# Kernel tuning notes

Hardware: AMD Instinct MI355X
Metric: run time of the kernel (lower is better)

Reference implementation:

```python
import jax, jax.numpy as jnp
import numpy as np

N_NODES = 40000
N_EDGES = 640000
NUM_GRAPHS = 64
NODE_DIM = 128
EDGE_DIM = 32
HID = 64
AGG_HID = 128
NEG_SLOPE = 0.2


def _segment_softmax(logits, seg, num_segments):
    # logits: [E, H], seg: [E] target-node index. Numerically stable per-segment softmax.
    m = jax.ops.segment_max(logits, seg, num_segments=num_segments)
    m = jnp.where(jnp.isfinite(m), m, 0.0)  # empty segments -> -inf max
    e = jnp.exp(logits - m[seg])
    denom = jax.ops.segment_sum(e, seg, num_segments=num_segments)
    return e / (denom[seg] + 1e-16)


def gatv2_conv(x, edge_index, edge_attr, Wl, bl, Wr, br, We, att, bias, concat):
    # PyG GATv2Conv with edge features (share_weights=False, lin_edge bias-free).
    N = x.shape[0]
    H, C = att.shape
    src, dst = edge_index[0], edge_index[1]
    xl = (x @ Wl + bl).reshape(N, H, C)          # lin_l(x) -> source transform
    xr = (x @ Wr + br).reshape(N, H, C)          # lin_r(x) -> target transform
    ee = (edge_attr @ We).reshape(-1, H, C)       # lin_edge(edge_attr)
    m = jax.nn.leaky_relu(xl[src] + xr[dst] + ee, NEG_SLOPE)  # [E,H,C]
    logits = jnp.einsum('ehc,hc->eh', m, att)     # [E,H]
    alpha = _segment_softmax(logits, dst, N)      # softmax over incoming edges
    out = jax.ops.segment_sum(xl[src] * alpha[..., None], dst, num_segments=N)  # [N,H,C]
    out = out.reshape(N, H * C) if concat else out.mean(axis=1)
    return out + bias


def setup_inputs() -> dict:
    key = jax.random.key(0)
    ks = iter(jax.random.split(key, 40))
    rn = lambda shape, s=0.1: (jax.random.normal(next(ks), shape, dtype=jnp.float32) * s)
    inp = {}
    inp['x'] = jax.random.normal(next(ks), (N_NODES, NODE_DIM), dtype=jnp.float32)
    inp['edge_attr'] = jax.random.normal(next(ks), (N_EDGES, EDGE_DIM), dtype=jnp.float32)
    inp['edge_index'] = jax.random.randint(next(ks), (2, N_EDGES), 0, N_NODES, dtype=jnp.int32)
    inp['batch'] = jnp.sort(jax.random.randint(next(ks), (N_NODES,), 0, NUM_GRAPHS, dtype=jnp.int32))
    inp.update(W1l=rn((NODE_DIM, 2 * HID)), b1l=jnp.zeros((2 * HID,), jnp.float32),
               W1r=rn((NODE_DIM, 2 * HID)), b1r=jnp.zeros((2 * HID,), jnp.float32),
               W1e=rn((EDGE_DIM, 2 * HID)), att1=rn((2, HID)), bias1=jnp.zeros((2 * HID,), jnp.float32))
    inp.update(W2l=rn((2 * HID, 2 * HID)), b2l=jnp.zeros((2 * HID,), jnp.float32),
               W2r=rn((2 * HID, 2 * HID)), b2r=jnp.zeros((2 * HID,), jnp.float32),
               W2e=rn((EDGE_DIM, 2 * HID)), att2=rn((2, HID)), bias2=jnp.zeros((2 * HID,), jnp.float32))
    # conv3: 128 -> 64, 1 head, concat=False
    inp.update(W3l=rn((2 * HID, HID)), b3l=jnp.zeros((HID,), jnp.float32),
               W3r=rn((2 * HID, HID)), b3r=jnp.zeros((HID,), jnp.float32),
               W3e=rn((EDGE_DIM, HID)), att3=rn((1, HID)), bias3=jnp.zeros((HID,), jnp.float32))
    inp.update(G1w=rn((HID, AGG_HID)), G1b=jnp.zeros((AGG_HID,), jnp.float32),
               G2w=rn((AGG_HID, 1)), G2b=jnp.zeros((1,), jnp.float32),
               Wreg=rn((HID, 1)), breg=jnp.zeros((1,), jnp.float32))
    return inp


def reference(x, edge_attr, edge_index, batch,
              W1l, b1l, W1r, b1r, W1e, att1, bias1,
              W2l, b2l, W2r, b2r, W2e, att2, bias2,
              W3l, b3l, W3r, b3r, W3e, att3, bias3,
              G1w, G1b, G2w, G2b, Wreg, breg):
    h = jax.nn.relu(gatv2_conv(x, edge_index, edge_attr, W1l, b1l, W1r, b1r, W1e, att1, bias1, True))
    h = jax.nn.relu(gatv2_conv(h, edge_index, edge_attr, W2l, b2l, W2r, b2r, W2e, att2, bias2, True))
    h = gatv2_conv(h, edge_index, edge_attr, W3l, b3l, W3r, b3r, W3e, att3, bias3, False)  # [N, HID]
    # Attentional aggregation over nodes, per graph
    gate = (jax.nn.relu(h @ G1w + G1b) @ G2w + G2b)[:, 0]            # [N]
    gate = _segment_softmax(gate[:, None], batch, NUM_GRAPHS)[:, 0]   # softmax within each graph
    pooled = jax.ops.segment_sum(gate[:, None] * h, batch, num_segments=NUM_GRAPHS)  # [B, HID]
    return (pooled @ Wreg + breg).squeeze(-1)  # [B]
```

## Files before the change

### kernel.cpp

```cpp
#include <hip/hip_runtime.h>

__global__ void k_fill(unsigned* p, int n, unsigned v) {
    int i = blockIdx.x * blockDim.x + threadIdx.x;
    if (i < n) p[i] = v;
}

__global__ void k_hist(const int* __restrict__ ei, int E, int* __restrict__ deg) {
    int e = blockIdx.x * blockDim.x + threadIdx.x;
    if (e < E) atomicAdd(&deg[ei[E + e]], 1);
}

__global__ void k_scan_blocks(const int* __restrict__ deg, int N,
                              int* __restrict__ excl, int* __restrict__ parts) {
    __shared__ int s[256];
    int t = threadIdx.x, i = blockIdx.x * 256 + t;
    int v = (i < N) ? deg[i] : 0;
    s[t] = v;
    __syncthreads();
    int acc = v;
    for (int off = 1; off < 256; off <<= 1) {
        int add = (t >= off) ? s[t - off] : 0;
        __syncthreads();
        acc += add;
        s[t] = acc;
        __syncthreads();
    }
    if (i < N) excl[i] = acc - v;
    if (t == 255) parts[blockIdx.x] = acc;
}

__global__ void k_scan_parts(int* __restrict__ parts, int nb) {
    __shared__ int s[256];
    int t = threadIdx.x;
    int v = (t < nb) ? parts[t] : 0;
    s[t] = v;
    __syncthreads();
    int acc = v;
    for (int off = 1; off < 256; off <<= 1) {
        int add = (t >= off) ? s[t - off] : 0;
        __syncthreads();
        acc += add;
        s[t] = acc;
        __syncthreads();
    }
    if (t < nb) parts[t] = acc - v;
}

__global__ void k_scan_add(const int* __restrict__ excl, const int* __restrict__ parts,
                           int* __restrict__ row_ptr, int* __restrict__ cursor, int N) {
    int i = blockIdx.x * blockDim.x + threadIdx.x;
    if (i >= N) return;
    int r = excl[i] + parts[i >> 8];
    row_ptr[i] = r;
    cursor[i] = r;
}

__global__ void k_scatter(const int* __restrict__ ei, int E, int* __restrict__ cursor,
                          int2* __restrict__ elist) {
    int e = blockIdx.x * blockDim.x + threadIdx.x;
    if (e >= E) return;
    int d = ei[E + e];
    int j = atomicAdd(&cursor[d], 1);
    elist[j] = make_int2(ei[e], e);
}

__global__ void k_reorder(const int2* __restrict__ elist, const float* __restrict__ ea, int E,
                          float4* __restrict__ ea_s) {
    int idx = blockIdx.x * blockDim.x + threadIdx.x;
    int j = idx >> 3, q = idx & 7;
    if (j >= E) return;
    ea_s[(size_t)j * 8 + q] = ((const float4*)ea)[(size_t)elist[j].y * 8 + q];
}

template <int M, int RW>
__global__ __launch_bounds__(256) void k_gemm2(const float* __restrict__ A,
                                               const float* __restrict__ Wl, const float* __restrict__ bl,
                                               const float* __restrict__ Wr, const float* __restrict__ br,
                                               float* __restrict__ outl, float* __restrict__ outr) {
    constexpr int TX = M / 4;
    __shared__ float sA[32][68];
    __shared__ float sW[32][M];
    const float* W    = blockIdx.y ? Wr : Wl;
    const float* bias = blockIdx.y ? br : bl;
    float* out        = blockIdx.y ? outr : outl;
    int t = threadIdx.x;
    int tx = t % TX, ty = t / TX;
    int r0 = blockIdx.x * 64;
    float acc[RW][4] = {};
    for (int kt = 0; kt < 128; kt += 32) {
        for (int l = t; l < 512; l += 256) {
            int row = l >> 3, kq = (l & 7) << 2;
            float4 a = *(const float4*)&A[(size_t)(r0 + row) * 128 + kt + kq];
            sA[kq + 0][row] = a.x; sA[kq + 1][row] = a.y;
            sA[kq + 2][row] = a.z; sA[kq + 3][row] = a.w;
        }
        for (int l = t; l < 32 * M / 4; l += 256) {
            int kk = (l * 4) / M, cc = (l * 4) % M;
            *(float4*)&sW[kk][cc] = *(const float4*)&W[(size_t)(kt + kk) * M + cc];
        }
        __syncthreads();
#pragma unroll
        for (int k = 0; k < 32; k++) {
            float4 w = *(float4*)&sW[k][tx * 4];
            float ar[RW];
#pragma unroll
            for (int i = 0; i < RW; i += 4) {
                float4 a = *(float4*)&sA[k][ty * RW + i];
                ar[i] = a.x; ar[i + 1] = a.y; ar[i + 2] = a.z; ar[i + 3] = a.w;
            }
#pragma unroll
            for (int i = 0; i < RW; i++) {
                acc[i][0] += ar[i] * w.x; acc[i][1] += ar[i] * w.y;
                acc[i][2] += ar[i] * w.z; acc[i][3] += ar[i] * w.w;
            }
        }
        __syncthreads();
    }
    float4 b = *(const float4*)&bias[tx * 4];
#pragma unroll
    for (int i = 0; i < RW; i++) {
        float4 v;
        v.x = acc[i][0] + b.x; v.y = acc[i][1] + b.y;
        v.z = acc[i][2] + b.z; v.w = acc[i][3] + b.w;
        *(float4*)&out[(size_t)(r0 + ty * RW + i) * M + tx * 4] = v;
    }
}

template <int H, bool RELU, bool SORTED>
__global__ __launch_bounds__(256) void k_agg(const float* __restrict__ xl, const float* __restrict__ xr,
                                             const float* __restrict__ ea, const float4* __restrict__ ea_s,
                                             const int2* __restrict__ elist,
                                             const int* __restrict__ row_ptr, const int* __restrict__ deg,
                                             const float* __restrict__ We, const float* __restrict__ att,
                                             const float* __restrict__ bias, float* __restrict__ out, int N) {
    constexpr int HC = H * 64;
    int tid = threadIdx.x, wv = tid >> 6, lane = tid & 63;
    float rWe0[32], rWe1[H == 2 ? 32 : 1];
#pragma unroll
    for (int k = 0; k < 32; k++) rWe0[k] = We[k * HC + lane];
    if constexpr (H == 2) {
#pragma unroll
        for (int k = 0; k < 32; k++) rWe1[k] = We[k * HC + 64 + lane];
    }
    float att0 = att[lane], b0 = bias[lane];
    float att1 = 0.f, b1 = 0.f;
    if constexpr (H == 2) { att1 = att[64 + lane]; b1 = bias[64 + lane]; }
    int n = blockIdx.x * 4 + wv;
    if (n >= N) return;
    int start = row_ptr[n], d = deg[n];
    float xr0 = xr[(size_t)n * HC + lane];
    float xr1 = (H == 2) ? xr[(size_t)n * HC + 64 + lane] : 0.f;
    float acc0 = 0.f, acc1 = 0.f, den0 = 0.f, den1 = 0.f;
    for (int j = 0; j < d; j++) {
        int2 sp = elist[start + j];
        const float4* eap = SORTED ? (ea_s + (size_t)(start + j) * 8)
                                   : (const float4*)(ea + (size_t)sp.y * 32);
        const float* xls = xl + (size_t)sp.x * HC;
        float xl0 = xls[lane];
        float xl1 = (H == 2) ? xls[64 + lane] : 0.f;
        float ee0 = 0.f, ee1 = 0.f;
#pragma unroll
        for (int kq = 0; kq < 8; kq++) {
            float4 v = eap[kq];
            ee0 = fmaf(v.x, rWe0[kq * 4 + 0], ee0);
            ee0 = fmaf(v.y, rWe0[kq * 4 + 1], ee0);
            ee0 = fmaf(v.z, rWe0[kq * 4 + 2], ee0);
            ee0 = fmaf(v.w, rWe0[kq * 4 + 3], ee0);
            if constexpr (H == 2) {
                ee1 = fmaf(v.x, rWe1[kq * 4 + 0], ee1);
                ee1 = fmaf(v.y, rWe1[kq * 4 + 1], ee1);
                ee1 = fmaf(v.z, rWe1[kq * 4 + 2], ee1);
                ee1 = fmaf(v.w, rWe1[kq * 4 + 3], ee1);
            }
        }
        float v0 = xl0 + xr0 + ee0;
        v0 = v0 > 0.f ? v0 : 0.2f * v0;
        float p0 = att0 * v0, p1 = 0.f;
        if constexpr (H == 2) {
            float v1 = xl1 + xr1 + ee1;
            v1 = v1 > 0.f ? v1 : 0.2f * v1;
            p1 = att1 * v1;
        }
#pragma unroll
        for (int m = 32; m; m >>= 1) {
            p0 += __shfl_xor(p0, m);
            if constexpr (H == 2) p1 += __shfl_xor(p1, m);
        }
        float ex0 = __expf(p0);
        acc0 = fmaf(ex0, xl0, acc0);
        den0 += ex0;
        if constexpr (H == 2) {
            float ex1 = __expf(p1);
            acc1 = fmaf(ex1, xl1, acc1);
            den1 += ex1;
        }
    }
    float o0 = acc0 / (den0 + 1e-16f) + b0;
    if (RELU) o0 = o0 > 0.f ? o0 : 0.f;
    out[(size_t)n * HC + lane] = o0;
    if constexpr (H == 2) {
        float o1 = acc1 / (den1 + 1e-16f) + b1;
        if (RELU) o1 = o1 > 0.f ? o1 : 0.f;
        out[(size_t)n * HC + 64 + lane] = o1;
    }
}

__global__ __launch_bounds__(256) void k_gate(const float* __restrict__ h, const float* __restrict__ G1w,
                                              const float* __restrict__ G1b, const float* __restrict__ G2w,
                                              const float* __restrict__ G2b,
                                              float* __restrict__ gate, int N) {
    __shared__ float sH[64][64];
    __shared__ float part[64][2];
    int t = threadIdx.x;
    int n0 = blockIdx.x * 64;
    for (int l = t; l < 1024; l += 256) {
        float4 v = ((const float4*)(h + (size_t)n0 * 64))[l];
        int n = l >> 4, kq = (l & 15) << 2;
        *(float4*)&sH[n][kq] = v;
    }
    int c = t & 127, half = t >> 7;
    float rW[64];
#pragma unroll
    for (int k = 0; k < 64; k++) rW[k] = G1w[k * 128 + c];
    float g1b = G1b[c], g2w = G2w[c];
    __syncthreads();
    for (int nn = 0; nn < 32; nn++) {
        int n = half * 32 + nn;
        float acc = g1b;
#pragma unroll
        for (int k = 0; k < 64; k += 4) {
            float4 hv = *(const float4*)&sH[n][k];
            acc = fmaf(hv.x, rW[k], acc);
            acc = fmaf(hv.y, rW[k + 1], acc);
            acc = fmaf(hv.z, rW[k + 2], acc);
            acc = fmaf(hv.w, rW[k + 3], acc);
        }
        acc = acc > 0.f ? acc : 0.f;
        float p = acc * g2w;
#pragma unroll
        for (int m = 32; m; m >>= 1) p += __shfl_xor(p, m);
        if ((t & 63) == 0) part[n][(t >> 6) & 1] = p;
    }
    __syncthreads();
    if (t < 64) gate[n0 + t] = __expf(part[t][0] + part[t][1] + G2b[0]);
}

__global__ __launch_bounds__(256) void k_pool(const float* __restrict__ h, const float* __restrict__ gate,
                                              const int* __restrict__ batch,
                                              float* __restrict__ pooled, int N) {
    int g = blockIdx.x;
    int lo = 0, hi = N;
    while (lo < hi) { int mid = (lo + hi) >> 1; if (batch[mid] < g) lo = mid + 1; else hi = mid; }
    int start = lo;
    lo = 0; hi = N;
    while (lo < hi) { int mid = (lo + hi) >> 1; if (batch[mid] < g + 1) lo = mid + 1; else hi = mid; }
    int end = lo;
    int t = threadIdx.x, wv = t >> 6, lane = t & 63;
    float acc = 0.f, den = 0.f;
    for (int n = start + wv; n < end; n += 4) {
        float gv = gate[n];
        acc = fmaf(gv, h[(size_t)n * 64 + lane], acc);
        den += gv;
    }
    __shared__ float sacc[4][64];
    __shared__ float sden[4];
    sacc[wv][lane] = acc;
    if (lane == 0) sden[wv] = den;
    __syncthreads();
    if (wv == 0) {
        float a = sacc[0][lane] + sacc[1][lane] + sacc[2][lane] + sacc[3][lane];
        float d = sden[0] + sden[1] + sden[2] + sden[3] + 1e-16f;
        pooled[g * 64 + lane] = a / d;
    }
}

__global__ void k_final(const float* __restrict__ pooled, const float* __restrict__ Wreg,
                        const float* __restrict__ breg, float* __restrict__ out) {
    int g = threadIdx.x;
    float acc = breg[0];
    for (int c = 0; c < 64; c++) acc += pooled[g * 64 + c] * Wreg[c];
    out[g] = acc;
}

extern "C" void kernel_launch(void* const* d_in, const int* in_sizes, int n_in,
                              void* d_out, int out_size, void* d_ws, size_t ws_size,
                              hipStream_t stream) {
    const float* x  = (const float*)d_in[0];
    const float* ea = (const float*)d_in[1];
    const int* ei    = (const int*)d_in[2];
    const int* batch = (const int*)d_in[3];
    auto ff = [&](int i) { return (const float*)d_in[i]; };
    const float *W1l = ff(4), *b1l = ff(5), *W1r = ff(6), *b1r = ff(7), *W1e = ff(8),
                *att1 = ff(9), *bias1 = ff(10);
    const float *W2l = ff(11), *b2l = ff(12), *W2r = ff(13), *b2r = ff(14), *W2e = ff(15),
                *att2 = ff(16), *bias2 = ff(17);
    const float *W3l = ff(18), *b3l = ff(19), *W3r = ff(20), *b3r = ff(21), *W3e = ff(22),
                *att3 = ff(23), *bias3 = ff(24);
    const float *G1w = ff(25), *G1b = ff(26), *G2w = ff(27), *G2b = ff(28), *Wreg = ff(29),
                *breg = ff(30);

    const int N = in_sizes[0] / 128;
    const int E = in_sizes[2] / 2;

    char* ws = (char*)d_ws;
    float*  bufA    = (float*)(ws);
    float*  bufB    = (float*)(ws + 20480000);
    float*  bufH    = (float*)(ws + 40960000);
    int2*   elist   = (int2*)(ws + 61440000);
    int*    row_ptr = (int*)(ws + 66560000);
    int*    deg     = (int*)(ws + 66720000);
    int*    cursor  = (int*)(ws + 66880000);
    int*    excl    = (int*)(ws + 67040000);
    int*    parts   = (int*)(ws + 67200000);
    float*  gate    = (float*)(ws + 67204096);
    float*  pooled  = (float*)(ws + 67364096);
    float4* ea_s    = (float4*)(ws + 67380480);
    const bool sorted_ea = ws_size >= (size_t)67380480 + (size_t)E * 32 * 4;

    auto cdiv = [](int a, int b) { return (a + b - 1) / b; };
    const int NB = cdiv(N, 256);
    const dim3 gemmG(N / 64, 2);
    const int AGGB = cdiv(N, 4);

    k_fill<<<NB, 256, 0, stream>>>((unsigned*)deg, N, 0u);
    k_hist<<<cdiv(E, 256), 256, 0, stream>>>(ei, E, deg);
    k_scan_blocks<<<NB, 256, 0, stream>>>(deg, N, excl, parts);
    k_scan_parts<<<1, 256, 0, stream>>>(parts, NB);
    k_scan_add<<<NB, 256, 0, stream>>>(excl, parts, row_ptr, cursor, N);
    k_scatter<<<cdiv(E, 256), 256, 0, stream>>>(ei, E, cursor, elist);
    if (sorted_ea)
        k_reorder<<<cdiv(E * 8, 256), 256, 0, stream>>>(elist, ea, E, ea_s);

    k_gemm2<128, 8><<<gemmG, 256, 0, stream>>>(x, W1l, b1l, W1r, b1r, bufA, bufB);
    if (sorted_ea)
        k_agg<2, true, true><<<AGGB, 256, 0, stream>>>(bufA, bufB, ea, ea_s, elist, row_ptr, deg, W1e, att1, bias1, bufH, N);
    else
        k_agg<2, true, false><<<AGGB, 256, 0, stream>>>(bufA, bufB, ea, ea_s, elist, row_ptr, deg, W1e, att1, bias1, bufH, N);

    k_gemm2<128, 8><<<gemmG, 256, 0, stream>>>(bufH, W2l, b2l, W2r, b2r, bufA, bufB);
    if (sorted_ea)
        k_agg<2, true, true><<<AGGB, 256, 0, stream>>>(bufA, bufB, ea, ea_s, elist, row_ptr, deg, W2e, att2, bias2, bufH, N);
    else
        k_agg<2, true, false><<<AGGB, 256, 0, stream>>>(bufA, bufB, ea, ea_s, elist, row_ptr, deg, W2e, att2, bias2, bufH, N);

    k_gemm2<64, 4><<<gemmG, 256, 0, stream>>>(bufH, W3l, b3l, W3r, b3r, bufA, bufB);
    if (sorted_ea)
        k_agg<1, false, true><<<AGGB, 256, 0, stream>>>(bufA, bufB, ea, ea_s, elist, row_ptr, deg, W3e, att3, bias3, bufH, N);
    else
        k_agg<1, false, false><<<AGGB, 256, 0, stream>>>(bufA, bufB, ea, ea_s, elist, row_ptr, deg, W3e, att3, bias3, bufH, N);

    k_gate<<<N / 64, 256, 0, stream>>>(bufH, G1w, G1b, G2w, G2b, gate, N);
    k_pool<<<64, 256, 0, stream>>>(bufH, gate, batch, pooled, N);
    k_final<<<1, 64, 0, stream>>>(pooled, Wreg, breg, (float*)d_out);
}
```

Baseline: 1.069 ms.

## Split attention heads across wavefronts and unroll edge loop by two in GATv2 aggregation

Result: slower. 1.898 ms (+77.6%).

```diff
diff --git a/kernel.cpp b/kernel.cpp
--- a/kernel.cpp
+++ b/kernel.cpp
@@ -126,83 +126,93 @@
     }
 }
 
-template <int H, bool RELU, bool SORTED>
+template <int HC, bool RELU, bool SORTED>
 __global__ __launch_bounds__(256) void k_agg(const float* __restrict__ xl, const float* __restrict__ xr,
                                              const float* __restrict__ ea, const float4* __restrict__ ea_s,
                                              const int2* __restrict__ elist,
                                              const int* __restrict__ row_ptr, const int* __restrict__ deg,
                                              const float* __restrict__ We, const float* __restrict__ att,
                                              const float* __restrict__ bias, float* __restrict__ out, int N) {
-    constexpr int HC = H * 64;
     int tid = threadIdx.x, wv = tid >> 6, lane = tid & 63;
-    float rWe0[32], rWe1[H == 2 ? 32 : 1];
-#pragma unroll
-    for (int k = 0; k < 32; k++) rWe0[k] = We[k * HC + lane];
-    if constexpr (H == 2) {
-#pragma unroll
-        for (int k = 0; k < 32; k++) rWe1[k] = We[k * HC + 64 + lane];
-    }
-    float att0 = att[lane], b0 = bias[lane];
-    float att1 = 0.f, b1 = 0.f;
-    if constexpr (H == 2) { att1 = att[64 + lane]; b1 = bias[64 + lane]; }
-    int n = blockIdx.x * 4 + wv;
+    int n, col;
+    if constexpr (HC == 128) {
+        n = blockIdx.x * 2 + (wv >> 1);
+        col = ((wv & 1) << 6) | lane;
+    } else {
+        n = blockIdx.x * 4 + wv;
+        col = lane;
+    }
+    float rWe[32];
+#pragma unroll
+    for (int k = 0; k < 32; k++) rWe[k] = We[k * HC + col];
+    float attc = att[col], bc = bias[col];
     if (n >= N) return;
     int start = row_ptr[n], d = deg[n];
-    float xr0 = xr[(size_t)n * HC + lane];
-    float xr1 = (H == 2) ? xr[(size_t)n * HC + 64 + lane] : 0.f;
-    float acc0 = 0.f, acc1 = 0.f, den0 = 0.f, den1 = 0.f;
-    for (int j = 0; j < d; j++) {
+    float xrc = xr[(size_t)n * HC + col];
+    float acc = 0.f, den = 0.f;
+    int j = 0;
+    for (; j + 2 <= d; j += 2) {
+        int2 spA = elist[start + j];
+        int2 spB = elist[start + j + 1];
+        const float4* eapA = SORTED ? (ea_s + (size_t)(start + j) * 8)
+                                    : (const float4*)(ea + (size_t)spA.y * 32);
+        const float4* eapB = SORTED ? (ea_s + (size_t)(start + j + 1) * 8)
+                                    : (const float4*)(ea + (size_t)spB.y * 32);
+        float xlA = xl[(size_t)spA.x * HC + col];
+        float xlB = xl[(size_t)spB.x * HC + col];
+        float eeA = 0.f, eeB = 0.f;
+#pragma unroll
+        for (int kq = 0; kq < 8; kq++) {
+            float4 va = eapA[kq];
+            float4 vb = eapB[kq];
+            eeA = fmaf(va.x, rWe[kq * 4 + 0], eeA);
+            eeA = fmaf(va.y, rWe[kq * 4 + 1], eeA);
+            eeA = fmaf(va.z, rWe[kq * 4 + 2], eeA);
+            eeA = fmaf(va.w, rWe[kq * 4 + 3], eeA);
+            eeB = fmaf(vb.x, rWe[kq * 4 + 0], eeB);
+            eeB = fmaf(vb.y, rWe[kq * 4 + 1], eeB);
+            eeB = fmaf(vb.z, rWe[kq * 4 + 2], eeB);
+            eeB = fmaf(vb.w, rWe[kq * 4 + 3], eeB);
+        }
+        float vA = xlA + xrc + eeA;
+        vA = vA > 0.f ? vA : 0.2f * vA;
+        float vB = xlB + xrc + eeB;
+        vB = vB > 0.f ? vB : 0.2f * vB;
+        float pA = attc * vA, pB = attc * vB;
+#pragma unroll
+        for (int m = 32; m; m >>= 1) {
+            pA += __shfl_xor(pA, m);
+            pB += __shfl_xor(pB, m);
+        }
+        float exA = __expf(pA), exB = __expf(pB);
+        acc = fmaf(exA, xlA, acc); den += exA;
+        acc = fmaf(exB, xlB, acc); den += exB;
+    }
+    if (j < d) {
         int2 sp = elist[start + j];
         const float4* eap = SORTED ? (ea_s + (size_t)(start + j) * 8)
                                    : (const float4*)(ea + (size_t)sp.y * 32);
-        const float* xls = xl + (size_t)sp.x * HC;
-        float xl0 = xls[lane];
-        float xl1 = (H == 2) ? xls[64 + lane] : 0.f;
-        float ee0 = 0.f, ee1 = 0.f;
+        float xlA = xl[(size_t)sp.x * HC + col];
+        float ee = 0.f;
 #pragma unroll
         for (int kq = 0; kq < 8; kq++) {
             float4 v = eap[kq];
-            ee0 = fmaf(v.x, rWe0[kq * 4 + 0], ee0);
-            ee0 = fmaf(v.y, rWe0[kq * 4 + 1], ee0);
-            ee0 = fmaf(v.z, rWe0[kq * 4 + 2], ee0);
-            ee0 = fmaf(v.w, rWe0[kq * 4 + 3], ee0);
-            if constexpr (H == 2) {
-                ee1 = fmaf(v.x, rWe1[kq * 4 + 0], ee1);
-                ee1 = fmaf(v.y, rWe1[kq * 4 + 1], ee1);
-                ee1 = fmaf(v.z, rWe1[kq * 4 + 2], ee1);
-                ee1 = fmaf(v.w, rWe1[kq * 4 + 3], ee1);
-            }
-        }
-        float v0 = xl0 + xr0 + ee0;
-        v0 = v0 > 0.f ? v0 : 0.2f * v0;
-        float p0 = att0 * v0, p1 = 0.f;
-        if constexpr (H == 2) {
-            float v1 = xl1 + xr1 + ee1;
-            v1 = v1 > 0.f ? v1 : 0.2f * v1;
-            p1 = att1 * v1;
-        }
-#pragma unroll
-        for (int m = 32; m; m >>= 1) {
-            p0 += __shfl_xor(p0, m);
-            if constexpr (H == 2) p1 += __shfl_xor(p1, m);
-        }
-        float ex0 = __expf(p0);
-        acc0 = fmaf(ex0, xl0, acc0);
-        den0 += ex0;
-        if constexpr (H == 2) {
-            float ex1 = __expf(p1);
-            acc1 = fmaf(ex1, xl1, acc1);
-            den1 += ex1;
-        }
-    }
-    float o0 = acc0 / (den0 + 1e-16f) + b0;
-    if (RELU) o0 = o0 > 0.f ? o0 : 0.f;
-    out[(size_t)n * HC + lane] = o0;
-    if constexpr (H == 2) {
-        float o1 = acc1 / (den1 + 1e-16f) + b1;
-        if (RELU) o1 = o1 > 0.f ? o1 : 0.f;
-        out[(size_t)n * HC + 64 + lane] = o1;
-    }
+            ee = fmaf(v.x, rWe[kq * 4 + 0], ee);
+            ee = fmaf(v.y, rWe[kq * 4 + 1], ee);
+            ee = fmaf(v.z, rWe[kq * 4 + 2], ee);
+            ee = fmaf(v.w, rWe[kq * 4 + 3], ee);
+        }
+        float v = xlA + xrc + ee;
+        v = v > 0.f ? v : 0.2f * v;
+        float p = attc * v;
+#pragma unroll
+        for (int m = 32; m; m >>= 1) p += __shfl_xor(p, m);
+        float ex = __expf(p);
+        acc = fmaf(ex, xlA, acc); den += ex;
+    }
+    float o = acc / (den + 1e-16f) + bc;
+    if (RELU) o = o > 0.f ? o : 0.f;
+    out[(size_t)n * HC + col] = o;
 }
 
 __global__ __launch_bounds__(256) void k_gate(const float* __restrict__ h, const float* __restrict__ G1w,
@@ -320,7 +330,6 @@
     auto cdiv = [](int a, int b) { return (a + b - 1) / b; };
     const int NB = cdiv(N, 256);
     const dim3 gemmG(N / 64, 2);
-    const int AGGB = cdiv(N, 4);
 
     k_fill<<<NB, 256, 0, stream>>>((unsigned*)deg, N, 0u);
     k_hist<<<cdiv(E, 256), 256, 0, stream>>>(ei, E, deg);
@@ -333,21 +342,21 @@
 
     k_gemm2<128, 8><<<gemmG, 256, 0, stream>>>(x, W1l, b1l, W1r, b1r, bufA, bufB);
     if (sorted_ea)
-        k_agg<2, true, true><<<AGGB, 256, 0, stream>>>(bufA, bufB, ea, ea_s, elist, row_ptr, deg, W1e, att1, bias1, bufH, N);
+        k_agg<128, true, true><<<cdiv(N, 2), 256, 0, stream>>>(bufA, bufB, ea, ea_s, elist, row_ptr, deg, W1e, att1, bias1, bufH, N);
     else
-        k_agg<2, true, false><<<AGGB, 256, 0, stream>>>(bufA, bufB, ea, ea_s, elist, row_ptr, deg, W1e, att1, bias1, bufH, N);
+        k_agg<128, true, false><<<cdiv(N, 2), 256, 0, stream>>>(bufA, bufB, ea, ea_s, elist, row_ptr, deg, W1e, att1, bias1, bufH, N);
 
     k_gemm2<128, 8><<<gemmG, 256, 0, stream>>>(bufH, W2l, b2l, W2r, b2r, bufA, bufB);
     if (sorted_ea)
-        k_agg<2, true, true><<<AGGB, 256, 0, stream>>>(bufA, bufB, ea, ea_s, elist, row_ptr, deg, W2e, att2, bias2, bufH, N);
+        k_agg<128, true, true><<<cdiv(N, 2), 256, 0, stream>>>(bufA, bufB, ea, ea_s, elist, row_ptr, deg, W2e, att2, bias2, bufH, N);
     else
-        k_agg<2, true, false><<<AGGB, 256, 0, stream>>>(bufA, bufB, ea, ea_s, elist, row_ptr, deg, W2e, att2, bias2, bufH, N);
+        k_agg<128, true, false><<<cdiv(N, 2), 256, 0, stream>>>(bufA, bufB, ea, ea_s, elist, row_ptr, deg, W2e, att2, bias2, bufH, N);
 
     k_gemm2<64, 4><<<gemmG, 256, 0, stream>>>(bufH, W3l, b3l, W3r, b3r, bufA, bufB);
     if (sorted_ea)
-        k_agg<1, false, true><<<AGGB, 256, 0, stream>>>(bufA, bufB, ea, ea_s, elist, row_ptr, deg, W3e, att3, bias3, bufH, N);
+        k_agg<64, false, true><<<cdiv(N, 4), 256, 0, stream>>>(bufA, bufB, ea, ea_s, elist, row_ptr, deg, W3e, att3, bias3, bufH, N);
     else
-        k_agg<1, false, false><<<AGGB, 256, 0, stream>>>(bufA, bufB, ea, ea_s, elist, row_ptr, deg, W3e, att3, bias3, bufH, N);
+        k_agg<64, false, false><<<cdiv(N, 4), 256, 0, stream>>>(bufA, bufB, ea, ea_s, elist, row_ptr, deg, W3e, att3, bias3, bufH, N);
 
     k_gate<<<N / 64, 256, 0, stream>>>(bufH, G1w, G1b, G2w, G2b, gate, N);
     k_pool<<<64, 256, 0, stream>>>(bufH, gate, batch, pooled, N);
```

## Remap aggregation lanes so each wave half owns one head

Applied to the files above, without the earlier changes.

Result: slower. 1.614 ms (+51.0%).

```diff
diff --git a/kernel.cpp b/kernel.cpp
--- a/kernel.cpp
+++ b/kernel.cpp
@@ -126,82 +126,135 @@
     }
 }
 
-template <int H, bool RELU, bool SORTED>
-__global__ __launch_bounds__(256) void k_agg(const float* __restrict__ xl, const float* __restrict__ xr,
-                                             const float* __restrict__ ea, const float4* __restrict__ ea_s,
-                                             const int2* __restrict__ elist,
-                                             const int* __restrict__ row_ptr, const int* __restrict__ deg,
-                                             const float* __restrict__ We, const float* __restrict__ att,
-                                             const float* __restrict__ bias, float* __restrict__ out, int N) {
-    constexpr int HC = H * 64;
+template <bool RELU, bool SORTED>
+__global__ __launch_bounds__(256) void k_agg2(const float* __restrict__ xl, const float* __restrict__ xr,
+                                              const float* __restrict__ ea, const float4* __restrict__ ea_s,
+                                              const int2* __restrict__ elist,
+                                              const int* __restrict__ row_ptr, const int* __restrict__ deg,
+                                              const float* __restrict__ We, const float* __restrict__ att,
+                                              const float* __restrict__ bias, float* __restrict__ out, int N) {
     int tid = threadIdx.x, wv = tid >> 6, lane = tid & 63;
-    float rWe0[32], rWe1[H == 2 ? 32 : 1];
-#pragma unroll
-    for (int k = 0; k < 32; k++) rWe0[k] = We[k * HC + lane];
-    if constexpr (H == 2) {
-#pragma unroll
-        for (int k = 0; k < 32; k++) rWe1[k] = We[k * HC + 64 + lane];
-    }
-    float att0 = att[lane], b0 = bias[lane];
-    float att1 = 0.f, b1 = 0.f;
-    if constexpr (H == 2) { att1 = att[64 + lane]; b1 = bias[64 + lane]; }
+    int half = lane >> 5, s = lane & 31;
+    int c0 = half * 64 + s;
+    int c1 = c0 + 32;
+    float rWeA[32], rWeB[32];
+#pragma unroll
+    for (int k = 0; k < 32; k++) rWeA[k] = We[k * 128 + c0];
+#pragma unroll
+    for (int k = 0; k < 32; k++) rWeB[k] = We[k * 128 + c1];
+    float attA = att[c0], attB = att[c1], bA = bias[c0], bB = bias[c1];
     int n = blockIdx.x * 4 + wv;
     if (n >= N) return;
     int start = row_ptr[n], d = deg[n];
-    float xr0 = xr[(size_t)n * HC + lane];
-    float xr1 = (H == 2) ? xr[(size_t)n * HC + 64 + lane] : 0.f;
-    float acc0 = 0.f, acc1 = 0.f, den0 = 0.f, den1 = 0.f;
+    float xrA = xr[(size_t)n * 128 + c0];
+    float xrB = xr[(size_t)n * 128 + c1];
+    float accA = 0.f, accB = 0.f, den = 0.f;
     for (int j = 0; j < d; j++) {
         int2 sp = elist[start + j];
         const float4* eap = SORTED ? (ea_s + (size_t)(start + j) * 8)
                                    : (const float4*)(ea + (size_t)sp.y * 32);
-        const float* xls = xl + (size_t)sp.x * HC;
-        float xl0 = xls[lane];
-        float xl1 = (H == 2) ? xls[64 + lane] : 0.f;
-        float ee0 = 0.f, ee1 = 0.f;
+        const float* xls = xl + (size_t)sp.x * 128;
+        float xlA = xls[c0];
+        float xlB = xls[c1];
+        float eeA = 0.f, eeB = 0.f;
 #pragma unroll
         for (int kq = 0; kq < 8; kq++) {
             float4 v = eap[kq];
-            ee0 = fmaf(v.x, rWe0[kq * 4 + 0], ee0);
-            ee0 = fmaf(v.y, rWe0[kq * 4 + 1], ee0);
-            ee0 = fmaf(v.z, rWe0[kq * 4 + 2], ee0);
-            ee0 = fmaf(v.w, rWe0[kq * 4 + 3], ee0);
-            if constexpr (H == 2) {
-                ee1 = fmaf(v.x, rWe1[kq * 4 + 0], ee1);
-                ee1 = fmaf(v.y, rWe1[kq * 4 + 1], ee1);
-                ee1 = fmaf(v.z, rWe1[kq * 4 + 2], ee1);
-                ee1 = fmaf(v.w, rWe1[kq * 4 + 3], ee1);
-            }
-        }
-        float v0 = xl0 + xr0 + ee0;
-        v0 = v0 > 0.f ? v0 : 0.2f * v0;
-        float p0 = att0 * v0, p1 = 0.f;
-        if constexpr (H == 2) {
-            float v1 = xl1 + xr1 + ee1;
-            v1 = v1 > 0.f ? v1 : 0.2f * v1;
-            p1 = att1 * v1;
-        }
-#pragma unroll
-        for (int m = 32; m; m >>= 1) {
-            p0 += __shfl_xor(p0, m);
-            if constexpr (H == 2) p1 += __shfl_xor(p1, m);
-        }
-        float ex0 = __expf(p0);
-        acc0 = fmaf(ex0, xl0, acc0);
-        den0 += ex0;
-        if constexpr (H == 2) {
-            float ex1 = __expf(p1);
-            acc1 = fmaf(ex1, xl1, acc1);
-            den1 += ex1;
-        }
-    }
-    float o0 = acc0 / (den0 + 1e-16f) + b0;
-    if (RELU) o0 = o0 > 0.f ? o0 : 0.f;
-    out[(size_t)n * HC + lane] = o0;
-    if constexpr (H == 2) {
-        float o1 = acc1 / (den1 + 1e-16f) + b1;
-        if (RELU) o1 = o1 > 0.f ? o1 : 0.f;
-        out[(size_t)n * HC + 64 + lane] = o1;
+            eeA = fmaf(v.x, rWeA[kq * 4 + 0], eeA);
+            eeA = fmaf(v.y, rWeA[kq * 4 + 1], eeA);
+            eeA = fmaf(v.z, rWeA[kq * 4 + 2], eeA);
+            eeA = fmaf(v.w, rWeA[kq * 4 + 3], eeA);
+            eeB = fmaf(v.x, rWeB[kq * 4 + 0], eeB);
+            eeB = fmaf(v.y, rWeB[kq * 4 + 1], eeB);
+            eeB = fmaf(v.z, rWeB[kq * 4 + 2], eeB);
+            eeB = fmaf(v.w, rWeB[kq * 4 + 3], eeB);
+        }
+        float vA = xlA + xrA + eeA;
+        vA = vA > 0.f ? vA : 0.2f * vA;
+        float vB = xlB + xrB + eeB;
+        vB = vB > 0.f ? vB : 0.2f * vB;
+        float p = fmaf(attA, vA, attB * vB);
+#pragma unroll
+        for (int m = 1; m <= 16; m <<= 1) p += __shfl_xor(p, m);
+        float ex = __expf(p);
+        accA = fmaf(ex, xlA, accA);
+        accB = fmaf(ex, xlB, accB);
+        den += ex;
+    }
+    float inv = 1.f / (den + 1e-16f);
+    float oA = fmaf(accA, inv, bA);
+    float oB = fmaf(accB, inv, bB);
+    if (RELU) { oA = oA > 0.f ? oA : 0.f; oB = oB > 0.f ? oB : 0.f; }
+    out[(size_t)n * 128 + c0] = oA;
+    out[(size_t)n * 128 + c1] = oB;
+}
+
+template <bool SORTED>
+__global__ __launch_bounds__(256) void k_agg1(const float* __restrict__ xl, const float* __restrict__ xr,
+                                              const float* __restrict__ ea, const float4* __restrict__ ea_s,
+                                              const int2* __restrict__ elist,
+                                              const int* __restrict__ row_ptr, const int* __restrict__ deg,
+                                              const float* __restrict__ We, const float* __restrict__ att,
+                                              const float* __restrict__ bias, float* __restrict__ out, int N) {
+    int tid = threadIdx.x, wv = tid >> 6, lane = tid & 63;
+    int half = lane >> 5, s = lane & 31;
+    int c0 = s, c1 = s + 32;
+    float rWeA[32], rWeB[32];
+#pragma unroll
+    for (int k = 0; k < 32; k++) rWeA[k] = We[k * 64 + c0];
+#pragma unroll
+    for (int k = 0; k < 32; k++) rWeB[k] = We[k * 64 + c1];
+    float attA = att[c0], attB = att[c1], bA = bias[c0], bB = bias[c1];
+    int n = blockIdx.x * 4 + wv;
+    if (n >= N) return;
+    int start = row_ptr[n], d = deg[n];
+    float xrA = xr[(size_t)n * 64 + c0];
+    float xrB = xr[(size_t)n * 64 + c1];
+    float accA = 0.f, accB = 0.f, den = 0.f;
+    for (int j = 0; j < d; j += 2) {
+        int jj = j + half;
+        bool valid = jj < d;
+        int idx = start + (valid ? jj : d - 1);
+        int2 sp = elist[idx];
+        const float4* eap = SORTED ? (ea_s + (size_t)idx * 8)
+                                   : (const float4*)(ea + (size_t)sp.y * 32);
+        const float* xls = xl + (size_t)sp.x * 64;
+        float xlA = xls[c0];
+        float xlB = xls[c1];
+        float eeA = 0.f, eeB = 0.f;
+#pragma unroll
+        for (int kq = 0; kq < 8; kq++) {
+            float4 v = eap[kq];
+            eeA = fmaf(v.x, rWeA[kq * 4 + 0], eeA);
+            eeA = fmaf(v.y, rWeA[kq * 4 + 1], eeA);
+            eeA = fmaf(v.z, rWeA[kq * 4 + 2], eeA);
+            eeA = fmaf(v.w, rWeA[kq * 4 + 3], eeA);
+            eeB = fmaf(v.x, rWeB[kq * 4 + 0], eeB);
+            eeB = fmaf(v.y, rWeB[kq * 4 + 1], eeB);
+            eeB = fmaf(v.z, rWeB[kq * 4 + 2], eeB);
+            eeB = fmaf(v.w, rWeB[kq * 4 + 3], eeB);
+        }
+        float vA = xlA + xrA + eeA;
+        vA = vA > 0.f ? vA : 0.2f * vA;
+        float vB = xlB + xrB + eeB;
+        vB = vB > 0.f ? vB : 0.2f * vB;
+        float p = fmaf(attA, vA, attB * vB);
+#pragma unroll
+        for (int m = 1; m <= 16; m <<= 1) p += __shfl_xor(p, m);
+        float ex = valid ? __expf(p) : 0.f;
+        accA = fmaf(ex, xlA, accA);
+        accB = fmaf(ex, xlB, accB);
+        den += ex;
+    }
+    accA += __shfl_xor(accA, 32);
+    accB += __shfl_xor(accB, 32);
+    den  += __shfl_xor(den, 32);
+    float inv = 1.f / (den + 1e-16f);
+    float oA = fmaf(accA, inv, bA);
+    float oB = fmaf(accB, inv, bB);
+    if (half == 0) {
+        out[(size_t)n * 64 + c0] = oA;
+        out[(size_t)n * 64 + c1] = oB;
     }
 }
 
@@ -333,21 +386,21 @@
 
     k_gemm2<128, 8><<<gemmG, 256, 0, stream>>>(x, W1l, b1l, W1r, b1r, bufA, bufB);
     if (sorted_ea)
-        k_agg<2, true, true><<<AGGB, 256, 0, stream>>>(bufA, bufB, ea, ea_s, elist, row_ptr, deg, W1e, att1, bias1, bufH, N);
+        k_agg2<true, true><<<AGGB, 256, 0, stream>>>(bufA, bufB, ea, ea_s, elist, row_ptr, deg, W1e, att1, bias1, bufH, N);
     else
-        k_agg<2, true, false><<<AGGB, 256, 0, stream>>>(bufA, bufB, ea, ea_s, elist, row_ptr, deg, W1e, att1, bias1, bufH, N);
+        k_agg2<true, false><<<AGGB, 256, 0, stream>>>(bufA, bufB, ea, ea_s, elist, row_ptr, deg, W1e, att1, bias1, bufH, N);
 
     k_gemm2<128, 8><<<gemmG, 256, 0, stream>>>(bufH, W2l, b2l, W2r, b2r, bufA, bufB);
     if (sorted_ea)
-        k_agg<2, true, true><<<AGGB, 256, 0, stream>>>(bufA, bufB, ea, ea_s, elist, row_ptr, deg, W2e, att2, bias2, bufH, N);
+        k_agg2<true, true><<<AGGB, 256, 0, stream>>>(bufA, bufB, ea, ea_s, elist, row_ptr, deg, W2e, att2, bias2, bufH, N);
     else
-        k_agg<2, true, false><<<AGGB, 256, 0, stream>>>(bufA, bufB, ea, ea_s, elist, row_ptr, deg, W2e, att2, bias2, bufH, N);
+        k_agg2<true, false><<<AGGB, 256, 0, stream>>>(bufA, bufB, ea, ea_s, elist, row_ptr, deg, W2e, att2, bias2, bufH, N);
 
     k_gemm2<64, 4><<<gemmG, 256, 0, stream>>>(bufH, W3l, b3l, W3r, b3r, bufA, bufB);
     if (sorted_ea)
-        k_agg<1, false, true><<<AGGB, 256, 0, stream>>>(bufA, bufB, ea, ea_s, elist, row_ptr, deg, W3e, att3, bias3, bufH, N);
+        k_agg1<true><<<AGGB, 256, 0, stream>>>(bufA, bufB, ea, ea_s, elist, row_ptr, deg, W3e, att3, bias3, bufH, N);
     else
-        k_agg<1, false, false><<<AGGB, 256, 0, stream>>>(bufA, bufB, ea, ea_s, elist, row_ptr, deg, W3e, att3, bias3, bufH, N);
+        k_agg1<false><<<AGGB, 256, 0, stream>>>(bufA, bufB, ea, ea_s, elist, row_ptr, deg, W3e, att3, bias3, bufH, N);
 
     k_gate<<<N / 64, 256, 0, stream>>>(bufH, G1w, G1b, G2w, G2b, gate, N);
     k_pool<<<64, 256, 0, stream>>>(bufH, gate, batch, pooled, N);
```
